# Optimization experiments

Measured on AMD Instinct MI355X. Metric: run time of the kernel, lower is better.

Reference implementation:

```python
import jax, jax.numpy as jnp
import numpy as np

NB = 31      # num_bands
PD = 64      # processing_dim


def _conv(x, w, b, groups, pad):
    # x: NCHW, w: OIHW (I = in_channels/groups)
    y = jax.lax.conv_general_dilated(
        x, w, window_strides=(1, 1), padding=pad,
        feature_group_count=groups,
        dimension_numbers=('NCHW', 'OIHW', 'NCHW'))
    return y + b[None, :, None, None]


def _gelu(z):
    # torch.nn.GELU() default is exact (erf-based)
    return jax.nn.gelu(z, approximate=False)


def setup_inputs() -> dict:
    key = jax.random.key(0)
    ks = jax.random.split(key, 11)
    s = 0.05
    inp = {
        'x':   jax.random.normal(ks[0], (2, NB, 192, 192), dtype=jnp.float32),
        # 31 independent band processors, stacked as grouped-conv weights (groups=31)
        'W1':  jax.random.normal(ks[1], (NB * PD, 1, 3, 3), dtype=jnp.float32) * s,
        'b1':  jax.random.normal(ks[2], (NB * PD,), dtype=jnp.float32) * s,
        'W2':  jax.random.normal(ks[3], (NB * PD, PD, 3, 3), dtype=jnp.float32) * s,
        'b2':  jax.random.normal(ks[4], (NB * PD,), dtype=jnp.float32) * s,
        'W3':  jax.random.normal(ks[5], (NB, PD, 1, 1), dtype=jnp.float32) * s,
        'b3':  jax.random.normal(ks[6], (NB,), dtype=jnp.float32) * s,
        # cross-band fusion 1x1 convs
        'Wf1': jax.random.normal(ks[7], (NB * 2, NB, 1, 1), dtype=jnp.float32) * s,
        'bf1': jax.random.normal(ks[8], (NB * 2,), dtype=jnp.float32) * s,
        'Wf2': jax.random.normal(ks[9], (NB, NB * 2, 1, 1), dtype=jnp.float32) * s,
        'bf2': jax.random.normal(ks[10], (NB,), dtype=jnp.float32) * s,
    }
    return inp


def reference(x, W1, b1, W2, b2, W3, b3, Wf1, bf1, Wf2, bf2):
    P3 = [(1, 1), (1, 1)]
    P1 = [(0, 0), (0, 0)]
    # per-band 3-layer stacks expressed as grouped convs (groups = num_bands)
    h = _gelu(_conv(x, W1, b1, NB, P3))           # [B, 31*64, H, W]
    h = _gelu(_conv(h, W2, b2, NB, P3))           # [B, 31*64, H, W]
    processed = _conv(h, W3, b3, NB, P1)          # [B, 31, H, W]
    # cross-band fusion
    f = _gelu(_conv(processed, Wf1, bf1, 1, P1))  # [B, 62, H, W]
    fused = _conv(f, Wf2, bf2, 1, P1)             # [B, 31, H, W]
    return x + fused
```

## Files before the change

kernel.cpp:

```cpp
#include <hip/hip_runtime.h>
#include <hip/hip_bf16.h>

#define NB 31
#define PD 64

typedef __attribute__((ext_vector_type(8))) short short8;
typedef __attribute__((ext_vector_type(16))) float f32x16;
typedef __attribute__((ext_vector_type(8))) int int8v;

__device__ __forceinline__ float gelu_f(float x) {
    float y = x * x;
    float p = __builtin_fmaf(y, __builtin_fmaf(y, 0.0042294f, -0.056913f), 0.395442f);
    float phi;
    asm("v_fma_f32 %0, %1, %2, 0.5 clamp" : "=v"(phi) : "v"(x), "v"(p));
    return x * phi;
}

__device__ __forceinline__ unsigned int cvt_pk_bf16(float lo, float hi) {
    unsigned int r;
    asm("v_cvt_pk_bf16_f32 %0, %1, %2" : "=v"(r) : "v"(lo), "v"(hi));
    return r;
}

__device__ __forceinline__ unsigned int pk_fp8(float a, float b) {
    return (unsigned int)__builtin_amdgcn_cvt_pk_fp8_f32(a, b, 0, false);
}

__device__ __forceinline__ int8v mk8(uint4 a, uint4 b) {
    int8v r;
    r[0] = a.x; r[1] = a.y; r[2] = a.z; r[3] = a.w;
    r[4] = b.x; r[5] = b.y; r[6] = b.z; r[7] = b.w;
    return r;
}

__global__ void prep_w2(const float* __restrict__ W2, unsigned char* __restrict__ W2s) {
    int e = blockIdx.x * 256 + threadIdx.x;
    const int TOT = NB * 2 * 9 * 64;
    if (e >= TOT) return;
    int lane = e & 63;
    int tap  = (e >> 6) % 9;
    int gh   = e / (9 * 64);
    int g = gh >> 1, oh = gh & 1;
    int col = lane & 31, hi = lane >> 5;
    const float* wp = W2 + ((size_t)(g * 64 + oh * 32 + col) * 64 + hi * 32) * 9 + tap;
    uint4 q0, q1;
    unsigned int d[8];
#pragma unroll
    for (int i = 0; i < 8; ++i) {
        float f0 = wp[(4 * i + 0) * 9];
        float f1 = wp[(4 * i + 1) * 9];
        float f2 = wp[(4 * i + 2) * 9];
        float f3 = wp[(4 * i + 3) * 9];
        d[i] = pk_fp8(f0, f1) | (pk_fp8(f2, f3) << 16);
    }
    q0.x = d[0]; q0.y = d[1]; q0.z = d[2]; q0.w = d[3];
    q1.x = d[4]; q1.y = d[5]; q1.z = d[6]; q1.w = d[7];
    uint4* op = (uint4*)W2s + (size_t)e * 2;
    op[0] = q0; op[1] = q1;
}

__global__ __launch_bounds__(512, 5) void band_kernel(
    const float* __restrict__ x, const float* __restrict__ W1, const float* __restrict__ b1,
    const float* __restrict__ b2, const float* __restrict__ W3, const float* __restrict__ b3,
    const unsigned char* __restrict__ W2s, float* __restrict__ out)
{
    __shared__ float xs[20 * 20];
    __shared__ uint4 h1s[352 * 4];
    __shared__ float outs[2 * 256];

    const int tid = threadIdx.x;
    const int tx = blockIdx.x % 12, ty = blockIdx.x / 12;
    const int g = blockIdx.y, n = blockIdx.z;
    const int x0 = tx * 16, y0 = ty * 16;

    const int lane = tid & 63;
    const int wid  = tid >> 6;
    const int w4   = wid & 3;
    const int oh   = wid >> 2;
    const int hi   = lane >> 5;
    const int col  = lane & 31;

    const float* xg = x + (size_t)(n * NB + g) * 192 * 192;
    if (tid < 400) {
        int r = tid / 20, c = tid - r * 20;
        int gy = y0 + r - 2, gx = x0 + c - 2;
        float v = 0.f;
        if (gy >= 0 && gy < 192 && gx >= 0 && gx < 192) v = xg[gy * 192 + gx];
        xs[tid] = v;
    }

    short8 a1;
    {
        const float* wp = W1 + (size_t)(g * 64 + oh * 32 + col) * 9;
        uint4 bw = {0u, 0u, 0u, 0u};
        if (hi == 0) {
            bw.x = cvt_pk_bf16(wp[0], wp[1]);
            bw.y = cvt_pk_bf16(wp[2], wp[3]);
            bw.z = cvt_pk_bf16(wp[4], wp[5]);
            bw.w = cvt_pk_bf16(wp[6], wp[7]);
        } else {
            bw.x = cvt_pk_bf16(wp[8], b1[g * 64 + oh * 32 + col]);
        }
        a1 = __builtin_bit_cast(short8, bw);
    }
    __syncthreads();

    char* h1c = (char*)h1s;
#pragma unroll
    for (int it = 0; it < 3; ++it) {
        const int t = w4 + 4 * it;
        if (t < 11) {
            const int posr = t * 32 + col;
            const int pos  = posr < 324 ? posr : 323;
            int py = pos / 18, px = pos - py * 18;
            int gy = y0 + py - 1, gx = x0 + px - 1;
            unsigned int msk = (gy >= 0 && gy < 192 && gx >= 0 && gx < 192) ? 0xFFFFFFFFu : 0u;

            uint4 bw = {0u, 0u, 0u, 0u};
            if (hi == 0) {
                float xv[8];
#pragma unroll
                for (int j2 = 0; j2 < 8; ++j2)
                    xv[j2] = xs[(py + j2 / 3) * 20 + px + (j2 % 3)];
                bw.x = cvt_pk_bf16(xv[0], xv[1]);
                bw.y = cvt_pk_bf16(xv[2], xv[3]);
                bw.z = cvt_pk_bf16(xv[4], xv[5]);
                bw.w = cvt_pk_bf16(xv[6], xv[7]);
            } else {
                bw.x = cvt_pk_bf16(xs[(py + 2) * 20 + px + 2], 1.0f);
            }
            short8 bfrag = __builtin_bit_cast(short8, bw);

            f32x16 z = {};
            f32x16 c0 = __builtin_amdgcn_mfma_f32_32x32x16_bf16(a1, bfrag, z, 0, 0, 0);

            const int rowb = posr << 6;
            const int sw = posr & 3;
#pragma unroll
            for (int s = 0; s < 4; ++s) {
                float u0 = gelu_f(c0[4 * s + 0]);
                float u1 = gelu_f(c0[4 * s + 1]);
                float u2 = gelu_f(c0[4 * s + 2]);
                float u3 = gelu_f(c0[4 * s + 3]);
                unsigned int E = (pk_fp8(u0, u1) | (pk_fp8(u2, u3) << 16)) & msk;
                int slot = ((s & 2) | oh) ^ sw;
                *(unsigned int*)(h1c + rowb + (slot << 4) + ((s & 1) << 3) + (hi << 2)) = E;
            }
        }
    }
    __syncthreads();

    const int lhalf = (lane >> 4) & 1;
    const int pxl   = lane & 15;
    const int base0 = (4 * w4 + lhalf) * 18 + pxl;

    const int gh = g * 2 + oh;
    const uint4* ap = (const uint4*)W2s + (size_t)gh * 9 * 128 + lane * 2;

    f32x16 acc0, acc1;
    {
        const float* bp = b2 + g * 64 + oh * 32 + 4 * hi;
#pragma unroll
        for (int s = 0; s < 4; ++s) {
            float4 q = *(const float4*)(bp + 8 * s);
            acc0[4 * s + 0] = q.x; acc0[4 * s + 1] = q.y;
            acc0[4 * s + 2] = q.z; acc0[4 * s + 3] = q.w;
            acc1[4 * s + 0] = q.x; acc1[4 * s + 1] = q.y;
            acc1[4 * s + 2] = q.z; acc1[4 * s + 3] = q.w;
        }
    }

    uint4 Aq[3][2];
    Aq[0][0] = ap[0];   Aq[0][1] = ap[1];
    Aq[1][0] = ap[128]; Aq[1][1] = ap[129];

#pragma unroll
    for (int tap = 0; tap < 9; ++tap) {
        if (tap + 2 < 9) {
            Aq[(tap + 2) % 3][0] = ap[(tap + 2) * 128];
            Aq[(tap + 2) % 3][1] = ap[(tap + 2) * 128 + 1];
        }
        const int D = (tap / 3) * 18 + (tap % 3);
        const int p0 = base0 + D;
        const int p1 = p0 + 36;
        const uint4* r0 = (const uint4*)(h1c + (p0 << 6));
        const uint4* r1 = (const uint4*)(h1c + (p1 << 6));
        const int s0 = p0 & 3, s1 = p1 & 3;
        uint4 b0a = r0[hi ^ s0];
        uint4 b0b = r0[(2 | hi) ^ s0];
        uint4 b1a = r1[hi ^ s1];
        uint4 b1b = r1[(2 | hi) ^ s1];
        int8v A = mk8(Aq[tap % 3][0], Aq[tap % 3][1]);
        acc0 = __builtin_amdgcn_mfma_scale_f32_32x32x64_f8f6f4(
                   A, mk8(b0a, b0b), acc0, 0, 0, 0, 0x7F7F7F7F, 0, 0x7F7F7F7F);
        acc1 = __builtin_amdgcn_mfma_scale_f32_32x32x64_f8f6f4(
                   A, mk8(b1a, b1b), acc1, 0, 0, 0, 0x7F7F7F7F, 0, 0x7F7F7F7F);
    }

    float pa = 0.f, pb = 0.f;
    {
        const float* wp3 = W3 + g * 64 + oh * 32 + 4 * hi;
#pragma unroll
        for (int s = 0; s < 4; ++s) {
            float4 qa = *(const float4*)(wp3 + 8 * s);
            pa = __builtin_fmaf(qa.x, gelu_f(acc0[4 * s + 0]), pa);
            pa = __builtin_fmaf(qa.y, gelu_f(acc0[4 * s + 1]), pa);
            pa = __builtin_fmaf(qa.z, gelu_f(acc0[4 * s + 2]), pa);
            pa = __builtin_fmaf(qa.w, gelu_f(acc0[4 * s + 3]), pa);
            pb = __builtin_fmaf(qa.x, gelu_f(acc1[4 * s + 0]), pb);
            pb = __builtin_fmaf(qa.y, gelu_f(acc1[4 * s + 1]), pb);
            pb = __builtin_fmaf(qa.z, gelu_f(acc1[4 * s + 2]), pb);
            pb = __builtin_fmaf(qa.w, gelu_f(acc1[4 * s + 3]), pb);
        }
    }
    pa += __shfl_xor(pa, 32);
    pb += __shfl_xor(pb, 32);
    if (lane < 32) {
        outs[oh * 256 + w4 * 64 + lane]      = pa;
        outs[oh * 256 + w4 * 64 + 32 + lane] = pb;
    }
    __syncthreads();

    if (tid < 256) {
        float v = outs[tid] + outs[256 + tid] + b3[g];
        int py = 4 * (tid >> 6) + 2 * ((tid >> 5) & 1) + ((tid >> 4) & 1);
        int px = tid & 15;
        out[((size_t)(n * NB + g) * 192 + y0 + py) * 192 + x0 + px] = v;
    }
}

__global__ __launch_bounds__(256) void fuse_kernel(
    const float* __restrict__ x,
    const float* __restrict__ Wf1, const float* __restrict__ bf1,
    const float* __restrict__ Wf2, const float* __restrict__ bf2,
    float* __restrict__ out)
{
    const int tid = threadIdx.x;
    int p = blockIdx.x * 256 + tid;
    int nn = p / 36864, pix = p - nn * 36864;
    float* basep = out + (size_t)nn * NB * 36864 + pix;
    const float* xb = x + (size_t)nn * NB * 36864 + pix;

    float v[31];
#pragma unroll
    for (int c = 0; c < 31; ++c) v[c] = basep[(size_t)c * 36864];

    float fused[31];
#pragma unroll
    for (int c = 0; c < 31; ++c) fused[c] = bf2[c];

#pragma unroll 2
    for (int j = 0; j < 62; ++j) {
        float a = bf1[j];
#pragma unroll
        for (int c = 0; c < 31; ++c) a = __builtin_fmaf(Wf1[j * 31 + c], v[c], a);
        float fj = gelu_f(a);
#pragma unroll
        for (int c = 0; c < 31; ++c) fused[c] = __builtin_fmaf(Wf2[c * 62 + j], fj, fused[c]);
    }
#pragma unroll
    for (int c = 0; c < 31; ++c) basep[(size_t)c * 36864] = xb[(size_t)c * 36864] + fused[c];
}

extern "C" void kernel_launch(void* const* d_in, const int* in_sizes, int n_in,
                              void* d_out, int out_size, void* d_ws, size_t ws_size,
                              hipStream_t stream) {
    const float* x   = (const float*)d_in[0];
    const float* W1  = (const float*)d_in[1];
    const float* b1  = (const float*)d_in[2];
    const float* W2  = (const float*)d_in[3];
    const float* b2  = (const float*)d_in[4];
    const float* W3  = (const float*)d_in[5];
    const float* b3  = (const float*)d_in[6];
    const float* Wf1 = (const float*)d_in[7];
    const float* bf1 = (const float*)d_in[8];
    const float* Wf2 = (const float*)d_in[9];
    const float* bf2 = (const float*)d_in[10];
    float* out = (float*)d_out;
    unsigned char* W2s = (unsigned char*)d_ws;

    const int TOT = NB * 2 * 9 * 64;
    hipLaunchKernelGGL(prep_w2, dim3((TOT + 255) / 256), dim3(256), 0, stream, W2, W2s);
    hipLaunchKernelGGL(band_kernel, dim3(144, NB, 2), dim3(512), 0, stream,
                       x, W1, b1, b2, W3, b3, W2s, out);
    hipLaunchKernelGGL(fuse_kernel, dim3(288), dim3(256), 0, stream,
                       x, Wf1, bf1, Wf2, bf2, out);
}
```

Before: 184.1 us.

## Pad h1 LDS rows to 80 bytes and reorder fp8 K layout

Replaces the XOR-swizzled 64-byte-per-position h1 layout in shared memory with a padded 80-byte row stride. Each position's fp8 activations are now laid out contiguously per half-wave, so the writes become 8-byte stores and the reads become plain 16-byte loads. The prep kernel permutes W2's K ordering to match the new B-fragment byte order. Launch bounds are raised to 6 blocks per CU, which tightens the register budget, while the padding enlarges LDS use. Both could hurt occupancy or cause spills.

```diff
diff --git a/kernel.cpp b/kernel.cpp
--- a/kernel.cpp
+++ b/kernel.cpp
@@ -43,7 +43,6 @@
     int g = gh >> 1, oh = gh & 1;
     int col = lane & 31, hi = lane >> 5;
     const float* wp = W2 + ((size_t)(g * 64 + oh * 32 + col) * 64 + hi * 32) * 9 + tap;
-    uint4 q0, q1;
     unsigned int d[8];
 #pragma unroll
     for (int i = 0; i < 8; ++i) {
@@ -53,19 +52,20 @@
         float f3 = wp[(4 * i + 3) * 9];
         d[i] = pk_fp8(f0, f1) | (pk_fp8(f2, f3) << 16);
     }
-    q0.x = d[0]; q0.y = d[1]; q0.z = d[2]; q0.w = d[3];
-    q1.x = d[4]; q1.y = d[5]; q1.z = d[6]; q1.w = d[7];
+    uint4 q0, q1;
+    q0.x = d[0]; q0.y = d[2]; q0.z = d[1]; q0.w = d[3];
+    q1.x = d[4]; q1.y = d[6]; q1.z = d[5]; q1.w = d[7];
     uint4* op = (uint4*)W2s + (size_t)e * 2;
     op[0] = q0; op[1] = q1;
 }
 
-__global__ __launch_bounds__(512, 5) void band_kernel(
+__global__ __launch_bounds__(512, 6) void band_kernel(
     const float* __restrict__ x, const float* __restrict__ W1, const float* __restrict__ b1,
     const float* __restrict__ b2, const float* __restrict__ W3, const float* __restrict__ b3,
     const unsigned char* __restrict__ W2s, float* __restrict__ out)
 {
     __shared__ float xs[20 * 20];
-    __shared__ uint4 h1s[352 * 4];
+    __shared__ uint4 h1s[352 * 5];
     __shared__ float outs[2 * 256];
 
     const int tid = threadIdx.x;
@@ -134,17 +134,22 @@
             f32x16 z = {};
             f32x16 c0 = __builtin_amdgcn_mfma_f32_32x32x16_bf16(a1, bfrag, z, 0, 0, 0);
 
-            const int rowb = posr << 6;
-            const int sw = posr & 3;
-#pragma unroll
-            for (int s = 0; s < 4; ++s) {
-                float u0 = gelu_f(c0[4 * s + 0]);
-                float u1 = gelu_f(c0[4 * s + 1]);
-                float u2 = gelu_f(c0[4 * s + 2]);
-                float u3 = gelu_f(c0[4 * s + 3]);
-                unsigned int E = (pk_fp8(u0, u1) | (pk_fp8(u2, u3) << 16)) & msk;
-                int slot = ((s & 2) | oh) ^ sw;
-                *(unsigned int*)(h1c + rowb + (slot << 4) + ((s & 1) << 3) + (hi << 2)) = E;
+            const int rowb = posr * 80;
+#pragma unroll
+            for (int p2 = 0; p2 < 2; ++p2) {
+                const int s0 = 2 * p2, s1 = 2 * p2 + 1;
+                float u0 = gelu_f(c0[4 * s0 + 0]);
+                float u1 = gelu_f(c0[4 * s0 + 1]);
+                float u2 = gelu_f(c0[4 * s0 + 2]);
+                float u3 = gelu_f(c0[4 * s0 + 3]);
+                float v0 = gelu_f(c0[4 * s1 + 0]);
+                float v1 = gelu_f(c0[4 * s1 + 1]);
+                float v2 = gelu_f(c0[4 * s1 + 2]);
+                float v3 = gelu_f(c0[4 * s1 + 3]);
+                uint2 st;
+                st.x = (pk_fp8(u0, u1) | (pk_fp8(u2, u3) << 16)) & msk;
+                st.y = (pk_fp8(v0, v1) | (pk_fp8(v2, v3) << 16)) & msk;
+                *(uint2*)(h1c + rowb + ((2 * oh + p2) << 4) + (hi << 3)) = st;
             }
         }
     }
@@ -183,13 +188,12 @@
         const int D = (tap / 3) * 18 + (tap % 3);
         const int p0 = base0 + D;
         const int p1 = p0 + 36;
-        const uint4* r0 = (const uint4*)(h1c + (p0 << 6));
-        const uint4* r1 = (const uint4*)(h1c + (p1 << 6));
-        const int s0 = p0 & 3, s1 = p1 & 3;
-        uint4 b0a = r0[hi ^ s0];
-        uint4 b0b = r0[(2 | hi) ^ s0];
-        uint4 b1a = r1[hi ^ s1];
-        uint4 b1b = r1[(2 | hi) ^ s1];
+        const char* r0 = h1c + p0 * 80 + (hi << 5);
+        const char* r1 = h1c + p1 * 80 + (hi << 5);
+        uint4 b0a = *(const uint4*)(r0);
+        uint4 b0b = *(const uint4*)(r0 + 16);
+        uint4 b1a = *(const uint4*)(r1);
+        uint4 b1b = *(const uint4*)(r1 + 16);
         int8v A = mk8(Aq[tap % 3][0], Aq[tap % 3][1]);
         acc0 = __builtin_amdgcn_mfma_scale_f32_32x32x64_f8f6f4(
                    A, mk8(b0a, b0b), acc0, 0, 0, 0, 0x7F7F7F7F, 0, 0x7F7F7F7F);
```

New measurement: 239.2 us. +29.9%, slower.
